# Kernel tuning notes

Hardware: AMD Instinct MI355X
Metric: run time of the kernel (lower is better)

## Reference

```python
import jax, jax.numpy as jnp
import numpy as np

B, S, E, H = 8, 1024, 1024, 16
D = E // H  # head dimension = 64


def setup_inputs() -> dict:
    key = jax.random.key(0)
    ks = jax.random.split(key, 9)
    sc = 1.0 / np.sqrt(E)
    return {
        "q": jax.random.normal(ks[0], (B, S, E), dtype=jnp.float32),
        "Wq_w": jax.random.normal(ks[1], (E, E), dtype=jnp.float32) * sc,
        "Wq_b": jax.random.normal(ks[2], (E,), dtype=jnp.float32) * 0.01,
        "Wk_w": jax.random.normal(ks[3], (E, E), dtype=jnp.float32) * sc,
        "Wk_b": jax.random.normal(ks[4], (E,), dtype=jnp.float32) * 0.01,
        "Wv_w": jax.random.normal(ks[5], (E, E), dtype=jnp.float32) * sc,
        "Wv_b": jax.random.normal(ks[6], (E,), dtype=jnp.float32) * 0.01,
        "Wo_w": jax.random.normal(ks[7], (E, E), dtype=jnp.float32) * sc,
        "Wo_b": jax.random.normal(ks[8], (E,), dtype=jnp.float32) * 0.01,
    }


def reference(q, Wq_w, Wq_b, Wk_w, Wk_b, Wv_w, Wv_b, Wo_w, Wo_b):
    # Linear projections (torch Linear: x @ W.T + b)
    Q = q @ Wq_w.T + Wq_b
    K = q @ Wk_w.T + Wk_b  # self-attention: k = v = q
    V = q @ Wv_w.T + Wv_b
    # [B, S, E] -> [B, H, S, D]
    Q = Q.reshape(B, S, H, D).transpose(0, 2, 1, 3)
    K = K.reshape(B, S, H, D).transpose(0, 2, 1, 3)
    V = V.reshape(B, S, H, D).transpose(0, 2, 1, 3)
    # Scores [B, H, S, S], scaled by sqrt(head_dim)
    scores = jnp.einsum('bhqd,bhkd->bhqk', Q, K) / jnp.sqrt(jnp.float32(D))
    attn = jax.nn.softmax(scores, axis=-1)
    # dropout p=0.0 (eval mode) -> identity
    out = jnp.einsum('bhqk,bhkd->bhqd', attn, V)
    out = out.transpose(0, 2, 1, 3).reshape(B, S, E)
    out = out @ Wo_w.T + Wo_b
    return out, attn
```

## Files before the change

kernel.cpp:

```cpp
#include <hip/hip_runtime.h>

using bf16x8 = __attribute__((ext_vector_type(8))) __bf16;
using f32x4  = __attribute__((ext_vector_type(4))) float;

#define NE 1024

__device__ __forceinline__ unsigned short f2b(float f) {
    unsigned u = __builtin_bit_cast(unsigned, f);
    u = (u + 0x7FFFu + ((u >> 16) & 1u)) >> 16;
    return (unsigned short)u;
}

typedef __attribute__((address_space(1))) const void gvoid_t;
typedef __attribute__((address_space(3))) void lvoid_t;

__device__ __forceinline__ void stage128(const unsigned short* gbase, char* lds, int tid)
{
    const int w = tid >> 6, l = tid & 63;
    #pragma unroll
    for (int i = 0; i < 4; ++i) {
        int grp = i * 4 + w;
        int row = grp * 8 + (l >> 3);
        int srcb = ((l & 7) * 16) ^ ((l >> 3) << 4);
        const char* g = (const char*)(gbase + (size_t)row * NE) + srcb;
        char* d = lds + grp * 1024;
        __builtin_amdgcn_global_load_lds((gvoid_t*)g, (lvoid_t*)d, 16, 0, 0);
    }
}

__global__ __launch_bounds__(256)
void conv_bf16(const float* __restrict__ src, unsigned short* __restrict__ dst)
{
    size_t i = ((size_t)blockIdx.x * 256 + threadIdx.x) * 8;
    float4 a0 = *(const float4*)(src + i);
    float4 a1 = *(const float4*)(src + i + 4);
    uint4 p;
    p.x = f2b(a0.x) | ((unsigned)f2b(a0.y) << 16);
    p.y = f2b(a0.z) | ((unsigned)f2b(a0.w) << 16);
    p.z = f2b(a1.x) | ((unsigned)f2b(a1.y) << 16);
    p.w = f2b(a1.z) | ((unsigned)f2b(a1.w) << 16);
    *(uint4*)(dst + i) = p;
}

template<int MODE>
__global__ __launch_bounds__(256)
void proj_bt(const unsigned short* __restrict__ A, const unsigned short* __restrict__ W,
             const float* __restrict__ bias, void* __restrict__ outp)
{
    __shared__ char Asm[16384], Bsm[16384];
    const int tid  = threadIdx.x;
    const int lane = tid & 63;
    const int wid  = tid >> 6;
    const int wr = wid >> 1, wc = wid & 1;
    const int swz = (blockIdx.x & 7) * 64 + (blockIdx.x >> 3);
    const int rowbase = (swz >> 3) * 128;
    const int colbase = (swz & 7) * 128;
    f32x4 acc[4][4] = {};

    for (int kt = 0; kt < 16; ++kt) {
        __syncthreads();
        stage128(A + (size_t)rowbase * NE + kt * 64, Asm, tid);
        stage128(W + (size_t)colbase * NE + kt * 64, Bsm, tid);
        __syncthreads();
        #pragma unroll
        for (int ks = 0; ks < 2; ++ks) {
            const int kb = ks * 64 + (lane >> 4) * 16;
            bf16x8 af[4], bf[4];
            #pragma unroll
            for (int m = 0; m < 4; ++m) {
                int row = wr * 64 + m * 16 + (lane & 15);
                af[m] = *(const bf16x8*)(Asm + ((row * 128 + kb) ^ ((row & 7) << 4)));
            }
            #pragma unroll
            for (int n = 0; n < 4; ++n) {
                int row = wc * 64 + n * 16 + (lane & 15);
                bf[n] = *(const bf16x8*)(Bsm + ((row * 128 + kb) ^ ((row & 7) << 4)));
            }
            #pragma unroll
            for (int m = 0; m < 4; ++m)
                #pragma unroll
                for (int n = 0; n < 4; ++n)
                    acc[m][n] = __builtin_amdgcn_mfma_f32_16x16x32_bf16(af[m], bf[n], acc[m][n], 0, 0, 0);
        }
    }

    #pragma unroll
    for (int m = 0; m < 4; ++m) {
        #pragma unroll
        for (int n = 0; n < 4; ++n) {
            int col = colbase + wc * 64 + n * 16 + (lane & 15);
            float bv = bias[col];
            #pragma unroll
            for (int r = 0; r < 4; ++r) {
                int row = rowbase + wr * 64 + m * 16 + (lane >> 4) * 4 + r;
                float v = acc[m][n][r] + bv;
                if (MODE == 0) {
                    ((unsigned short*)outp)[(size_t)row * NE + col] = f2b(v);
                } else if (MODE == 1) {
                    int b = row >> 10, s = row & 1023, h = col >> 6, d = col & 63;
                    ((unsigned short*)outp)[((size_t)((b * 16 + h) * 64 + d) << 10) + s] = f2b(v);
                } else {
                    ((float*)outp)[(size_t)row * NE + col] = v;
                }
            }
        }
    }
}

__global__ __launch_bounds__(256)
void fused_attn(const unsigned short* __restrict__ Q,
                const unsigned short* __restrict__ K,
                const unsigned short* __restrict__ VT,
                float* __restrict__ attn, unsigned short* __restrict__ Og)
{
    __shared__ char Qsm[16384], Ksm[16384];
    __shared__ char Psm[32768];
    __shared__ float rs4[4][128];
    __shared__ float il[128];
    const int tid  = threadIdx.x;
    const int lane = tid & 63;
    const int w    = tid >> 6;
    const int swzb = (blockIdx.x & 7) * 128 + (blockIdx.x >> 3);
    const int bh = swzb >> 3, qt = swzb & 7;
    const int b = bh >> 4, h = bh & 15;
    const unsigned short* Qg = Q  + (size_t)(b * 1024 + qt * 128) * 1024 + h * 64;
    const unsigned short* Kg = K  + (size_t)(b * 1024) * 1024 + h * 64;
    const unsigned short* Vg = VT + (size_t)bh * 64 * 1024;

    stage128(Qg, Qsm, tid);

    float rs_p[8] = {0.f, 0.f, 0.f, 0.f, 0.f, 0.f, 0.f, 0.f};
    for (int kt = 0; kt < 8; ++kt) {
        __syncthreads();
        stage128(Kg + (size_t)(kt * 128) * 1024, Ksm, tid);
        __syncthreads();
        f32x4 sa[2][8] = {};
        #pragma unroll
        for (int ks = 0; ks < 2; ++ks) {
            const int kb = ks * 64 + (lane >> 4) * 16;
            bf16x8 kf[2], qf[8];
            #pragma unroll
            for (int m = 0; m < 2; ++m) {
                int row = w * 32 + m * 16 + (lane & 15);
                kf[m] = *(const bf16x8*)(Ksm + ((row * 128 + kb) ^ ((row & 7) << 4)));
            }
            #pragma unroll
            for (int n = 0; n < 8; ++n) {
                int row = n * 16 + (lane & 15);
                qf[n] = *(const bf16x8*)(Qsm + ((row * 128 + kb) ^ ((row & 7) << 4)));
            }
            #pragma unroll
            for (int m = 0; m < 2; ++m)
                #pragma unroll
                for (int n = 0; n < 8; ++n)
                    sa[m][n] = __builtin_amdgcn_mfma_f32_16x16x32_bf16(kf[m], qf[n], sa[m][n], 0, 0, 0);
        }
        #pragma unroll
        for (int n = 0; n < 8; ++n)
            #pragma unroll
            for (int m = 0; m < 2; ++m)
                #pragma unroll
                for (int r = 0; r < 4; ++r)
                    rs_p[n] += __expf(sa[m][n][r] * 0.125f - 8.0f);
    }
    #pragma unroll
    for (int n = 0; n < 8; ++n) {
        rs_p[n] += __shfl_xor(rs_p[n], 16);
        rs_p[n] += __shfl_xor(rs_p[n], 32);
    }
    if (lane < 16) {
        #pragma unroll
        for (int n = 0; n < 8; ++n) rs4[w][n * 16 + lane] = rs_p[n];
    }
    __syncthreads();
    if (tid < 128) il[tid] = 1.0f / (rs4[0][tid] + rs4[1][tid] + rs4[2][tid] + rs4[3][tid]);

    f32x4 oa[2][4] = {};
    float* attnq = attn + ((size_t)bh * 1024 + qt * 128) * 1024;
    for (int kt = 0; kt < 8; ++kt) {
        __syncthreads();
        stage128(Kg + (size_t)(kt * 128) * 1024, Ksm, tid);
        __syncthreads();
        f32x4 sa[2][8] = {};
        #pragma unroll
        for (int ks = 0; ks < 2; ++ks) {
            const int kb = ks * 64 + (lane >> 4) * 16;
            bf16x8 kf[2], qf[8];
            #pragma unroll
            for (int m = 0; m < 2; ++m) {
                int row = w * 32 + m * 16 + (lane & 15);
                kf[m] = *(const bf16x8*)(Ksm + ((row * 128 + kb) ^ ((row & 7) << 4)));
            }
            #pragma unroll
            for (int n = 0; n < 8; ++n) {
                int row = n * 16 + (lane & 15);
                qf[n] = *(const bf16x8*)(Qsm + ((row * 128 + kb) ^ ((row & 7) << 4)));
            }
            #pragma unroll
            for (int m = 0; m < 2; ++m)
                #pragma unroll
                for (int n = 0; n < 8; ++n)
                    sa[m][n] = __builtin_amdgcn_mfma_f32_16x16x32_bf16(kf[m], qf[n], sa[m][n], 0, 0, 0);
        }
        #pragma unroll
        for (int n = 0; n < 8; ++n) {
            int q = n * 16 + (lane & 15);
            float iv = il[q];
            #pragma unroll
            for (int m = 0; m < 2; ++m) {
                int k0 = w * 32 + m * 16 + (lane >> 4) * 4;
                float4 p4;
                p4.x = __expf(sa[m][n][0] * 0.125f - 8.0f) * iv;
                p4.y = __expf(sa[m][n][1] * 0.125f - 8.0f) * iv;
                p4.z = __expf(sa[m][n][2] * 0.125f - 8.0f) * iv;
                p4.w = __expf(sa[m][n][3] * 0.125f - 8.0f) * iv;
                *(float4*)(attnq + (size_t)q * 1024 + kt * 128 + k0) = p4;
                uint2 pk;
                pk.x = f2b(p4.x) | ((unsigned)f2b(p4.y) << 16);
                pk.y = f2b(p4.z) | ((unsigned)f2b(p4.w) << 16);
                int ad = (q * 256 + k0 * 2) ^ ((q & 7) << 4);
                *(uint2*)(Psm + ad) = pk;
            }
        }
        __syncthreads();
        #pragma unroll
        for (int ks = 0; ks < 4; ++ks) {
            const int kb = ks * 64 + (lane >> 4) * 16;
            bf16x8 pa[2], vb[4];
            #pragma unroll
            for (int m2 = 0; m2 < 2; ++m2) {
                int row = w * 32 + m2 * 16 + (lane & 15);
                pa[m2] = *(const bf16x8*)(Psm + ((row * 256 + kb) ^ ((row & 7) << 4)));
            }
            #pragma unroll
            for (int n2 = 0; n2 < 4; ++n2) {
                int d = n2 * 16 + (lane & 15);
                vb[n2] = *(const bf16x8*)(Vg + (size_t)d * 1024 + kt * 128 + ks * 32 + (lane >> 4) * 8);
            }
            #pragma unroll
            for (int m2 = 0; m2 < 2; ++m2)
                #pragma unroll
                for (int n2 = 0; n2 < 4; ++n2)
                    oa[m2][n2] = __builtin_amdgcn_mfma_f32_16x16x32_bf16(pa[m2], vb[n2], oa[m2][n2], 0, 0, 0);
        }
    }
    unsigned short* Ob = Og + (size_t)(b * 1024 + qt * 128) * 1024 + h * 64;
    #pragma unroll
    for (int m2 = 0; m2 < 2; ++m2)
        #pragma unroll
        for (int n2 = 0; n2 < 4; ++n2) {
            int d = n2 * 16 + (lane & 15);
            #pragma unroll
            for (int r = 0; r < 4; ++r) {
                int qrow = w * 32 + m2 * 16 + (lane >> 4) * 4 + r;
                Ob[(size_t)qrow * 1024 + d] = f2b(oa[m2][n2][r]);
            }
        }
}

extern "C" void kernel_launch(void* const* d_in, const int* in_sizes, int n_in,
                              void* d_out, int out_size, void* d_ws, size_t ws_size,
                              hipStream_t stream) {
    (void)in_sizes; (void)n_in; (void)out_size; (void)ws_size;
    const float* q    = (const float*)d_in[0];
    const float* Wq_w = (const float*)d_in[1];
    const float* Wq_b = (const float*)d_in[2];
    const float* Wk_w = (const float*)d_in[3];
    const float* Wk_b = (const float*)d_in[4];
    const float* Wv_w = (const float*)d_in[5];
    const float* Wv_b = (const float*)d_in[6];
    const float* Wo_w = (const float*)d_in[7];
    const float* Wo_b = (const float*)d_in[8];

    char* ws = (char*)d_ws;
    unsigned short* Qws  = (unsigned short*)(ws);
    unsigned short* Kws  = (unsigned short*)(ws + (16u << 20));
    unsigned short* VTws = (unsigned short*)(ws + (32u << 20));

    float* outp  = (float*)d_out;
    float* attnp = outp + 8388608;

    char* scr = (char*)attnp;
    unsigned short* qbf = (unsigned short*)scr;
    unsigned short* wqb = (unsigned short*)(scr + (16u << 20));
    unsigned short* wkb = (unsigned short*)(scr + (18u << 20));
    unsigned short* wvb = (unsigned short*)(scr + (20u << 20));

    dim3 blk(256);
    conv_bf16<<<dim3(4096), blk, 0, stream>>>(q, qbf);
    conv_bf16<<<dim3(512),  blk, 0, stream>>>(Wq_w, wqb);
    conv_bf16<<<dim3(512),  blk, 0, stream>>>(Wk_w, wkb);
    conv_bf16<<<dim3(512),  blk, 0, stream>>>(Wv_w, wvb);
    proj_bt<0><<<dim3(512), blk, 0, stream>>>(qbf, wqb, Wq_b, Qws);
    proj_bt<0><<<dim3(512), blk, 0, stream>>>(qbf, wkb, Wk_b, Kws);
    proj_bt<1><<<dim3(512), blk, 0, stream>>>(qbf, wvb, Wv_b, VTws);
    fused_attn<<<dim3(1024), blk, 0, stream>>>(Qws, Kws, VTws, attnp, Qws);
    conv_bf16<<<dim3(512),  blk, 0, stream>>>(Wo_w, Kws);
    proj_bt<2><<<dim3(512), blk, 0, stream>>>(Qws, Kws, Wo_b, outp);
}
```

Before: 338.3 us.

## Pipeline K staging, keep Q in registers, stage V in LDS, fold normalization into exp2

Q fragments are loaded once into registers instead of being reread from LDS on every tile. The next K tile is prefetched right after the QK MFMAs, which drops one barrier per iteration. V tiles are staged into swizzled LDS with async global-to-LDS loads instead of being read straight from global memory. Softmax uses exp2 with a folded log2 normalizer in place of a multiply by the reciprocal, and the MFMA sections are wrapped in setprio with launch bounds of 2 blocks per CU. Keeping Q in registers raises register pressure, and the occupancy hint may cause spills.

```diff
diff --git a/kernel.cpp b/kernel.cpp
--- a/kernel.cpp
+++ b/kernel.cpp
@@ -4,6 +4,8 @@
 using f32x4  = __attribute__((ext_vector_type(4))) float;
 
 #define NE 1024
+#define C1E 0.18033688011112042f
+#define C2E -11.541560327111707f
 
 __device__ __forceinline__ unsigned short f2b(float f) {
     unsigned u = __builtin_bit_cast(unsigned, f);
@@ -24,6 +26,20 @@
         int srcb = ((l & 7) * 16) ^ ((l >> 3) << 4);
         const char* g = (const char*)(gbase + (size_t)row * NE) + srcb;
         char* d = lds + grp * 1024;
+        __builtin_amdgcn_global_load_lds((gvoid_t*)g, (lvoid_t*)d, 16, 0, 0);
+    }
+}
+
+__device__ __forceinline__ void stage64x256(const unsigned short* gbase, char* lds, int tid)
+{
+    const int w = tid >> 6, l = tid & 63;
+    #pragma unroll
+    for (int i = 0; i < 4; ++i) {
+        int row0 = i * 16 + w * 4;
+        int row = row0 + (l >> 4);
+        int srcb = ((l & 15) * 16) ^ ((row & 7) << 4);
+        const char* g = (const char*)(gbase + (size_t)row * 1024) + srcb;
+        char* d = lds + row0 * 256;
         __builtin_amdgcn_global_load_lds((gvoid_t*)g, (lvoid_t*)d, 16, 0, 0);
     }
 }
@@ -107,16 +123,17 @@
     }
 }
 
-__global__ __launch_bounds__(256)
+__global__ __launch_bounds__(256, 2)
 void fused_attn(const unsigned short* __restrict__ Q,
                 const unsigned short* __restrict__ K,
                 const unsigned short* __restrict__ VT,
                 float* __restrict__ attn, unsigned short* __restrict__ Og)
 {
-    __shared__ char Qsm[16384], Ksm[16384];
+    __shared__ char Ksm[16384];
+    __shared__ char Vsm[16384];
     __shared__ char Psm[32768];
     __shared__ float rs4[4][128];
-    __shared__ float il[128];
+    __shared__ float lt[128];
     const int tid  = threadIdx.x;
     const int lane = tid & 63;
     const int w    = tid >> 6;
@@ -127,41 +144,50 @@
     const unsigned short* Kg = K  + (size_t)(b * 1024) * 1024 + h * 64;
     const unsigned short* Vg = VT + (size_t)bh * 64 * 1024;
 
-    stage128(Qg, Qsm, tid);
+    stage128(Qg, Psm, tid);
+    __syncthreads();
+    bf16x8 qf[2][8];
+    #pragma unroll
+    for (int ks = 0; ks < 2; ++ks) {
+        const int kb = ks * 64 + (lane >> 4) * 16;
+        #pragma unroll
+        for (int n = 0; n < 8; ++n) {
+            int row = n * 16 + (lane & 15);
+            qf[ks][n] = *(const bf16x8*)(Psm + ((row * 128 + kb) ^ ((row & 7) << 4)));
+        }
+    }
+    stage128(Kg, Ksm, tid);
 
     float rs_p[8] = {0.f, 0.f, 0.f, 0.f, 0.f, 0.f, 0.f, 0.f};
     for (int kt = 0; kt < 8; ++kt) {
         __syncthreads();
-        stage128(Kg + (size_t)(kt * 128) * 1024, Ksm, tid);
-        __syncthreads();
         f32x4 sa[2][8] = {};
+        __builtin_amdgcn_s_setprio(1);
         #pragma unroll
         for (int ks = 0; ks < 2; ++ks) {
             const int kb = ks * 64 + (lane >> 4) * 16;
-            bf16x8 kf[2], qf[8];
+            bf16x8 kf[2];
             #pragma unroll
             for (int m = 0; m < 2; ++m) {
                 int row = w * 32 + m * 16 + (lane & 15);
                 kf[m] = *(const bf16x8*)(Ksm + ((row * 128 + kb) ^ ((row & 7) << 4)));
             }
             #pragma unroll
-            for (int n = 0; n < 8; ++n) {
-                int row = n * 16 + (lane & 15);
-                qf[n] = *(const bf16x8*)(Qsm + ((row * 128 + kb) ^ ((row & 7) << 4)));
-            }
-            #pragma unroll
             for (int m = 0; m < 2; ++m)
                 #pragma unroll
                 for (int n = 0; n < 8; ++n)
-                    sa[m][n] = __builtin_amdgcn_mfma_f32_16x16x32_bf16(kf[m], qf[n], sa[m][n], 0, 0, 0);
-        }
+                    sa[m][n] = __builtin_amdgcn_mfma_f32_16x16x32_bf16(kf[m], qf[ks][n], sa[m][n], 0, 0, 0);
+        }
+        __builtin_amdgcn_s_setprio(0);
+        __syncthreads();
+        if (kt < 7) stage128(Kg + (size_t)((kt + 1) * 128) * 1024, Ksm, tid);
         #pragma unroll
         for (int n = 0; n < 8; ++n)
             #pragma unroll
             for (int m = 0; m < 2; ++m)
                 #pragma unroll
                 for (int r = 0; r < 4; ++r)
-                    rs_p[n] += __expf(sa[m][n][r] * 0.125f - 8.0f);
+                    rs_p[n] += exp2f(fmaf(sa[m][n][r], C1E, C2E));
     }
     #pragma unroll
     for (int n = 0; n < 8; ++n) {
@@ -173,56 +199,57 @@
         for (int n = 0; n < 8; ++n) rs4[w][n * 16 + lane] = rs_p[n];
     }
     __syncthreads();
-    if (tid < 128) il[tid] = 1.0f / (rs4[0][tid] + rs4[1][tid] + rs4[2][tid] + rs4[3][tid]);
+    if (tid < 128) {
+        float l = rs4[0][tid] + rs4[1][tid] + rs4[2][tid] + rs4[3][tid];
+        lt[tid] = C2E - __log2f(l);
+    }
+    stage128(Kg, Ksm, tid);
 
     f32x4 oa[2][4] = {};
     float* attnq = attn + ((size_t)bh * 1024 + qt * 128) * 1024;
     for (int kt = 0; kt < 8; ++kt) {
         __syncthreads();
-        stage128(Kg + (size_t)(kt * 128) * 1024, Ksm, tid);
-        __syncthreads();
+        stage64x256(Vg + kt * 128, Vsm, tid);
         f32x4 sa[2][8] = {};
+        __builtin_amdgcn_s_setprio(1);
         #pragma unroll
         for (int ks = 0; ks < 2; ++ks) {
             const int kb = ks * 64 + (lane >> 4) * 16;
-            bf16x8 kf[2], qf[8];
+            bf16x8 kf[2];
             #pragma unroll
             for (int m = 0; m < 2; ++m) {
                 int row = w * 32 + m * 16 + (lane & 15);
                 kf[m] = *(const bf16x8*)(Ksm + ((row * 128 + kb) ^ ((row & 7) << 4)));
             }
             #pragma unroll
-            for (int n = 0; n < 8; ++n) {
-                int row = n * 16 + (lane & 15);
-                qf[n] = *(const bf16x8*)(Qsm + ((row * 128 + kb) ^ ((row & 7) << 4)));
-            }
-            #pragma unroll
             for (int m = 0; m < 2; ++m)
                 #pragma unroll
                 for (int n = 0; n < 8; ++n)
-                    sa[m][n] = __builtin_amdgcn_mfma_f32_16x16x32_bf16(kf[m], qf[n], sa[m][n], 0, 0, 0);
-        }
+                    sa[m][n] = __builtin_amdgcn_mfma_f32_16x16x32_bf16(kf[m], qf[ks][n], sa[m][n], 0, 0, 0);
+        }
+        __builtin_amdgcn_s_setprio(0);
         #pragma unroll
         for (int n = 0; n < 8; ++n) {
             int q = n * 16 + (lane & 15);
-            float iv = il[q];
+            float ltq = lt[q];
             #pragma unroll
             for (int m = 0; m < 2; ++m) {
                 int k0 = w * 32 + m * 16 + (lane >> 4) * 4;
                 float4 p4;
-                p4.x = __expf(sa[m][n][0] * 0.125f - 8.0f) * iv;
-                p4.y = __expf(sa[m][n][1] * 0.125f - 8.0f) * iv;
-                p4.z = __expf(sa[m][n][2] * 0.125f - 8.0f) * iv;
-                p4.w = __expf(sa[m][n][3] * 0.125f - 8.0f) * iv;
+                p4.x = exp2f(fmaf(sa[m][n][0], C1E, ltq));
+                p4.y = exp2f(fmaf(sa[m][n][1], C1E, ltq));
+                p4.z = exp2f(fmaf(sa[m][n][2], C1E, ltq));
+                p4.w = exp2f(fmaf(sa[m][n][3], C1E, ltq));
                 *(float4*)(attnq + (size_t)q * 1024 + kt * 128 + k0) = p4;
                 uint2 pk;
                 pk.x = f2b(p4.x) | ((unsigned)f2b(p4.y) << 16);
                 pk.y = f2b(p4.z) | ((unsigned)f2b(p4.w) << 16);
-                int ad = (q * 256 + k0 * 2) ^ ((q & 7) << 4);
-                *(uint2*)(Psm + ad) = pk;
-            }
-        }
-        __syncthreads();
+                *(uint2*)(Psm + ((q * 256 + k0 * 2) ^ ((q & 7) << 4))) = pk;
+            }
+        }
+        __syncthreads();
+        if (kt < 7) stage128(Kg + (size_t)((kt + 1) * 128) * 1024, Ksm, tid);
+        __builtin_amdgcn_s_setprio(1);
         #pragma unroll
         for (int ks = 0; ks < 4; ++ks) {
             const int kb = ks * 64 + (lane >> 4) * 16;
@@ -235,7 +262,7 @@
             #pragma unroll
             for (int n2 = 0; n2 < 4; ++n2) {
                 int d = n2 * 16 + (lane & 15);
-                vb[n2] = *(const bf16x8*)(Vg + (size_t)d * 1024 + kt * 128 + ks * 32 + (lane >> 4) * 8);
+                vb[n2] = *(const bf16x8*)(Vsm + d * 256 + (kb ^ ((d & 7) << 4)));
             }
             #pragma unroll
             for (int m2 = 0; m2 < 2; ++m2)
@@ -243,6 +270,7 @@
                 for (int n2 = 0; n2 < 4; ++n2)
                     oa[m2][n2] = __builtin_amdgcn_mfma_f32_16x16x32_bf16(pa[m2], vb[n2], oa[m2][n2], 0, 0, 0);
         }
+        __builtin_amdgcn_s_setprio(0);
     }
     unsigned short* Ob = Og + (size_t)(b * 1024 + qt * 128) * 1024 + h * 64;
     #pragma unroll
```

Measured after the change: 287.5 us. 15.0% less time.
